# Performance work log

Hardware: AMD Instinct MI355X
Metric: run time of the kernel (lower is better)

Reference implementation:

```python
import jax, jax.numpy as jnp
import numpy as np

NUM_BINS = 64
MAX_DIST = 25.0
HIDDEN = 256
B = 64        # number of graphs
S = 1024      # points per graph (setup builds equal-size contiguous segments)
EPS = 1e-8


def setup_inputs() -> dict:
    key = jax.random.key(0)
    k1, k2, k3, k4, k5 = jax.random.split(key, 5)
    N = B * S
    # scale positions so pairwise distances spread across [0, 25] bins
    pos = jax.random.normal(k1, (N, 3), dtype=jnp.float32) * 5.0
    batch = jnp.repeat(jnp.arange(B, dtype=jnp.int32), S)  # sorted graph ids
    # nn.Linear params, torch convention W:[out,in]
    W1 = jax.random.normal(k2, (HIDDEN, NUM_BINS), dtype=jnp.float32) / np.sqrt(NUM_BINS)
    b1 = jax.random.normal(k3, (HIDDEN,), dtype=jnp.float32) * 0.01
    W2 = jax.random.normal(k4, (HIDDEN, HIDDEN), dtype=jnp.float32) / np.sqrt(HIDDEN)
    b2 = jax.random.normal(k5, (HIDDEN,), dtype=jnp.float32) * 0.01
    return {"pos": pos, "W1": W1, "b1": b1, "W2": W2, "b2": b2, "batch": batch}


def _histograms(pos, batch):
    # batch ids are contiguous equal-size segments -> reshape into [B,S,3]
    p = pos.reshape(B, S, 3)
    # pairwise distances per graph via gram trick (matches torch.cdist)
    sq = jnp.sum(p * p, axis=-1)                                  # [B,S]
    d2 = sq[:, :, None] + sq[:, None, :] - 2.0 * jnp.einsum("bsd,btd->bst", p, p)
    dist = jnp.sqrt(jnp.maximum(d2, 0.0))                         # [B,S,S]
    triu = jnp.triu(jnp.ones((S, S), dtype=bool), k=1)            # i<j pairs
    # histc semantics: values in [0, MAX_DIST] counted, value==MAX_DIST -> last bin
    valid = triu[None] & (dist <= MAX_DIST)
    bins = jnp.clip(jnp.floor(dist * (NUM_BINS / MAX_DIST)).astype(jnp.int32), 0, NUM_BINS - 1)
    ids = (jnp.arange(B, dtype=jnp.int32)[:, None, None] * NUM_BINS + bins).reshape(-1)
    hist = jax.ops.segment_sum(valid.astype(jnp.float32).reshape(-1), ids,
                               num_segments=B * NUM_BINS).reshape(B, NUM_BINS)
    return hist / (jnp.sum(hist, axis=-1, keepdims=True) + EPS)


def reference(pos, W1, b1, W2, b2, batch):
    hist = _histograms(pos, batch)                                # [B, NUM_BINS]
    h = jax.nn.silu(hist @ W1.T + b1)                             # [B, HIDDEN]
    return h @ W2.T + b2                                          # [B, HIDDEN]
```

## Files before the change

### kernel.cpp

```cpp
#include <hip/hip_runtime.h>

#define NBINS 64
#define NGRAPH 64
#define HID 256
#define TILE 128
#define NPAIR 36
#define BPG NPAIR
#define WSUB 16
#define NSUB 64
#define HSTR 65

__device__ __constant__ unsigned char ti_tab[NPAIR] = {
  0,0,0,0,0,0,0,0, 1,1,1,1,1,1,1, 2,2,2,2,2,2, 3,3,3,3,3, 4,4,4,4, 5,5,5, 6,6, 7};
__device__ __constant__ unsigned char tj_tab[NPAIR] = {
  0,1,2,3,4,5,6,7, 1,2,3,4,5,6,7, 2,3,4,5,6,7, 3,4,5,6,7, 4,5,6,7, 5,6,7, 6,7, 7};

template <bool OFFDIAG>
__device__ __forceinline__ void pair_loop(const float4* __restrict__ plj,
                                          unsigned int* __restrict__ hw,
                                          float4 pa, float4 pb, int il0, int il1,
                                          int jbase) {
  #pragma unroll 8
  for (int jj = 0; jj < 32; ++jj) {
    int jl = jbase + jj;
    float4 pj = plj[jl];
    float dxa = pa.x - pj.x, dya = pa.y - pj.y, dza = pa.z - pj.z;
    float d2a = dxa * dxa + dya * dya + dza * dza;
    float dxb = pb.x - pj.x, dyb = pb.y - pj.y, dzb = pb.z - pj.z;
    float d2b = dxb * dxb + dyb * dyb + dzb * dzb;
    unsigned int ia = (unsigned int)(int)__builtin_amdgcn_sqrtf(d2a);
    unsigned int ib = (unsigned int)(int)__builtin_amdgcn_sqrtf(d2b);
    ia = ia > 64u ? 64u : ia;
    ib = ib > 64u ? 64u : ib;
    if (!OFFDIAG) {
      ia = (il0 < jl) ? ia : 64u;
      ib = (il1 < jl) ? ib : 64u;
    }
    atomicAdd(&hw[ia], 1u);
    atomicAdd(&hw[ib], 1u);
  }
}

__global__ __launch_bounds__(256) void hist_kernel(const float* __restrict__ pos,
                                                   unsigned int* __restrict__ partial) {
  int bid = blockIdx.x;
  int g   = bid / NPAIR;
  int p   = bid - g * NPAIR;
  int ti  = ti_tab[p];
  int tj  = tj_tab[p];
  int t   = threadIdx.x;
  const float S = 2.56f;

  __shared__ float4 plj[TILE];
  __shared__ unsigned int h[NSUB * HSTR];

  #pragma unroll
  for (int k = t; k < NSUB * HSTR; k += 256) h[k] = 0u;
  if (t < TILE) {
    const float* gp = pos + (size_t)((g << 10) + (tj << 7) + t) * 3;
    plj[t] = make_float4(gp[0] * S, gp[1] * S, gp[2] * S, 0.0f);
  }

  int il0 = (t & 63) * 2;
  int il1 = il0 + 1;
  const float* ip = pos + (size_t)((g << 10) + (ti << 7) + il0) * 3;
  float4 pa = make_float4(ip[0] * S, ip[1] * S, ip[2] * S, 0.0f);
  float4 pb = make_float4(ip[3] * S, ip[4] * S, ip[5] * S, 0.0f);
  int jbase = (t >> 6) * 32;
  unsigned int* hw = h + ((t >> 6) * WSUB + (t & (WSUB - 1))) * HSTR;
  __syncthreads();

  if (ti != tj) pair_loop<true >(plj, hw, pa, pb, il0, il1, jbase);
  else          pair_loop<false>(plj, hw, pa, pb, il0, il1, jbase);
  __syncthreads();

  if (t < NBINS) {
    unsigned int s = 0u;
    #pragma unroll
    for (int k = 0; k < NSUB; ++k) s += h[k * HSTR + t];
    partial[(size_t)bid * NBINS + t] = s;
  }
}

__global__ __launch_bounds__(256) void mlp_kernel(const unsigned int* __restrict__ partial,
                                                  const float* __restrict__ W1,
                                                  const float* __restrict__ b1,
                                                  const float* __restrict__ W2,
                                                  const float* __restrict__ b2,
                                                  float* __restrict__ out) {
  int g = blockIdx.x >> 2;
  int q = blockIdx.x & 3;
  int t = threadIdx.x;
  __shared__ float hn[NBINS];
  __shared__ float h1[HID];
  __shared__ float p2[4][NBINS];

  if (t < NBINS) {
    unsigned int s = 0u;
    const unsigned int* pp = partial + (size_t)g * BPG * NBINS + t;
    #pragma unroll
    for (int p = 0; p < BPG; ++p) s += pp[p * NBINS];
    float hv = (float)s;
    float tot = hv;
    #pragma unroll
    for (int m = 1; m < 64; m <<= 1) tot += __shfl_xor(tot, m, 64);
    hn[t] = hv / (tot + 1e-8f);
  }
  __syncthreads();

  {
    float acc = b1[t];
    const float4* w = (const float4*)(W1 + (size_t)t * NBINS);
    #pragma unroll
    for (int k = 0; k < NBINS / 4; ++k) {
      float4 wv = w[k];
      acc += hn[4 * k] * wv.x + hn[4 * k + 1] * wv.y +
             hn[4 * k + 2] * wv.z + hn[4 * k + 3] * wv.w;
    }
    float sig = 1.0f / (1.0f + expf(-acc));
    h1[t] = acc * sig;
  }
  __syncthreads();

  {
    int o  = (q << 6) + (t & 63);
    int ks = (t >> 6) << 6;
    float acc = 0.0f;
    const float4* w = (const float4*)(W2 + (size_t)o * HID + ks);
    #pragma unroll
    for (int k = 0; k < 16; ++k) {
      float4 wv = w[k];
      acc += h1[ks + 4 * k] * wv.x + h1[ks + 4 * k + 1] * wv.y +
             h1[ks + 4 * k + 2] * wv.z + h1[ks + 4 * k + 3] * wv.w;
    }
    p2[t >> 6][t & 63] = acc;
  }
  __syncthreads();

  if (t < 64) {
    int o = (q << 6) + t;
    out[(size_t)g * HID + o] = b2[o] + p2[0][t] + p2[1][t] + p2[2][t] + p2[3][t];
  }
}

extern "C" void kernel_launch(void* const* d_in, const int* in_sizes, int n_in,
                              void* d_out, int out_size, void* d_ws, size_t ws_size,
                              hipStream_t stream) {
  const float* pos = (const float*)d_in[0];
  const float* W1  = (const float*)d_in[1];
  const float* b1  = (const float*)d_in[2];
  const float* W2  = (const float*)d_in[3];
  const float* b2  = (const float*)d_in[4];

  unsigned int* partial = (unsigned int*)d_ws;

  hipLaunchKernelGGL(hist_kernel, dim3(NGRAPH * BPG), dim3(256), 0, stream, pos, partial);
  hipLaunchKernelGGL(mlp_kernel, dim3(NGRAPH * 4), dim3(256), 0, stream,
                     partial, W1, b1, W2, b2, (float*)d_out);
}
```

Baseline: 86.32 us.

## Use 256x128 rectangular pair tiles with 4 i-points per thread

The histogram kernel switches from 36 square 128x128 upper-triangle tiles per graph to 20 rectangular tiles of 256 i-points by 128 j-points. Each thread now handles four i-points against each shared j-point, so every LDS load of a j-point is reused more. The i-point loads become three float4 vector loads. The per-block sub-histogram count is halved (32 copies instead of 64), which cuts init and reduction work but may raise atomic contention. The MLP kernel spreads the partial-histogram reduction across all four waves instead of one.

```diff
diff --git a/kernel.cpp b/kernel.cpp
--- a/kernel.cpp
+++ b/kernel.cpp
@@ -3,75 +3,75 @@
 #define NBINS 64
 #define NGRAPH 64
 #define HID 256
-#define TILE 128
-#define NPAIR 36
-#define BPG NPAIR
-#define WSUB 16
-#define NSUB 64
+#define TJ 128
+#define NBLK 20
+#define BPG NBLK
+#define PPW 5
+#define NSUB 32
 #define HSTR 65
 
-__device__ __constant__ unsigned char ti_tab[NPAIR] = {
-  0,0,0,0,0,0,0,0, 1,1,1,1,1,1,1, 2,2,2,2,2,2, 3,3,3,3,3, 4,4,4,4, 5,5,5, 6,6, 7};
-__device__ __constant__ unsigned char tj_tab[NPAIR] = {
-  0,1,2,3,4,5,6,7, 1,2,3,4,5,6,7, 2,3,4,5,6,7, 3,4,5,6,7, 4,5,6,7, 5,6,7, 6,7, 7};
+__device__ __constant__ unsigned char itab[NBLK] = {
+  0,0,0,0,0,0,0,0, 1,1,1,1,1,1, 2,2,2,2, 3,3};
+__device__ __constant__ unsigned char jtab[NBLK] = {
+  0,1,2,3,4,5,6,7, 2,3,4,5,6,7, 4,5,6,7, 6,7};
 
-template <bool OFFDIAG>
+template <bool FULL>
 __device__ __forceinline__ void pair_loop(const float4* __restrict__ plj,
                                           unsigned int* __restrict__ hw,
-                                          float4 pa, float4 pb, int il0, int il1,
-                                          int jbase) {
-  #pragma unroll 8
+                                          const float4* p, int irel, int jbase) {
+  #pragma unroll 4
   for (int jj = 0; jj < 32; ++jj) {
     int jl = jbase + jj;
     float4 pj = plj[jl];
-    float dxa = pa.x - pj.x, dya = pa.y - pj.y, dza = pa.z - pj.z;
-    float d2a = dxa * dxa + dya * dya + dza * dza;
-    float dxb = pb.x - pj.x, dyb = pb.y - pj.y, dzb = pb.z - pj.z;
-    float d2b = dxb * dxb + dyb * dyb + dzb * dzb;
-    unsigned int ia = (unsigned int)(int)__builtin_amdgcn_sqrtf(d2a);
-    unsigned int ib = (unsigned int)(int)__builtin_amdgcn_sqrtf(d2b);
-    ia = ia > 64u ? 64u : ia;
-    ib = ib > 64u ? 64u : ib;
-    if (!OFFDIAG) {
-      ia = (il0 < jl) ? ia : 64u;
-      ib = (il1 < jl) ? ib : 64u;
+    #pragma unroll
+    for (int m = 0; m < 4; ++m) {
+      float dx = p[m].x - pj.x, dy = p[m].y - pj.y, dz = p[m].z - pj.z;
+      float d2 = dx * dx + dy * dy + dz * dz;
+      unsigned int b = (unsigned int)(int)__builtin_amdgcn_sqrtf(d2);
+      b = b > 64u ? 64u : b;
+      if (!FULL) b = (irel + m < jl) ? b : 64u;
+      atomicAdd(&hw[b], 1u);
     }
-    atomicAdd(&hw[ia], 1u);
-    atomicAdd(&hw[ib], 1u);
   }
 }
 
 __global__ __launch_bounds__(256) void hist_kernel(const float* __restrict__ pos,
                                                    unsigned int* __restrict__ partial) {
   int bid = blockIdx.x;
-  int g   = bid / NPAIR;
-  int p   = bid - g * NPAIR;
-  int ti  = ti_tab[p];
-  int tj  = tj_tab[p];
+  int g   = bid / NBLK;
+  int p   = bid - g * NBLK;
+  int ti  = itab[p];
+  int tj  = jtab[p];
+  bool full = (tj >= 2 * ti + 2);
   int t   = threadIdx.x;
   const float S = 2.56f;
 
-  __shared__ float4 plj[TILE];
+  __shared__ float4 plj[TJ];
   __shared__ unsigned int h[NSUB * HSTR];
 
-  #pragma unroll
   for (int k = t; k < NSUB * HSTR; k += 256) h[k] = 0u;
-  if (t < TILE) {
+  if (t < TJ) {
     const float* gp = pos + (size_t)((g << 10) + (tj << 7) + t) * 3;
     plj[t] = make_float4(gp[0] * S, gp[1] * S, gp[2] * S, 0.0f);
   }
 
-  int il0 = (t & 63) * 2;
-  int il1 = il0 + 1;
-  const float* ip = pos + (size_t)((g << 10) + (ti << 7) + il0) * 3;
-  float4 pa = make_float4(ip[0] * S, ip[1] * S, ip[2] * S, 0.0f);
-  float4 pb = make_float4(ip[3] * S, ip[4] * S, ip[5] * S, 0.0f);
+  int il = (t & 63) << 2;
+  const float* ip = pos + (size_t)((g << 10) + (ti << 8) + il) * 3;
+  float4 A = *(const float4*)(ip);
+  float4 Bv = *(const float4*)(ip + 4);
+  float4 C = *(const float4*)(ip + 8);
+  float4 pp[4];
+  pp[0] = make_float4(A.x * S, A.y * S, A.z * S, 0.f);
+  pp[1] = make_float4(A.w * S, Bv.x * S, Bv.y * S, 0.f);
+  pp[2] = make_float4(Bv.z * S, Bv.w * S, C.x * S, 0.f);
+  pp[3] = make_float4(C.y * S, C.z * S, C.w * S, 0.f);
+  int irel  = (ti << 8) + il - (tj << 7);
   int jbase = (t >> 6) * 32;
-  unsigned int* hw = h + ((t >> 6) * WSUB + (t & (WSUB - 1))) * HSTR;
+  unsigned int* hw = h + ((t >> 6) * 8 + (t & 7)) * HSTR;
   __syncthreads();
 
-  if (ti != tj) pair_loop<true >(plj, hw, pa, pb, il0, il1, jbase);
-  else          pair_loop<false>(plj, hw, pa, pb, il0, il1, jbase);
+  if (full) pair_loop<true >(plj, hw, pp, irel, jbase);
+  else      pair_loop<false>(plj, hw, pp, irel, jbase);
   __syncthreads();
 
   if (t < NBINS) {
@@ -91,16 +91,22 @@
   int g = blockIdx.x >> 2;
   int q = blockIdx.x & 3;
   int t = threadIdx.x;
+  int w = t >> 6, l = t & 63;
+  __shared__ float psum[4][NBINS];
   __shared__ float hn[NBINS];
   __shared__ float h1[HID];
   __shared__ float p2[4][NBINS];
 
+  {
+    unsigned int s = 0u;
+    const unsigned int* pp = partial + (size_t)g * BPG * NBINS + l;
+    #pragma unroll
+    for (int k = 0; k < PPW; ++k) s += pp[(w * PPW + k) * NBINS];
+    psum[w][l] = (float)s;
+  }
+  __syncthreads();
   if (t < NBINS) {
-    unsigned int s = 0u;
-    const unsigned int* pp = partial + (size_t)g * BPG * NBINS + t;
-    #pragma unroll
-    for (int p = 0; p < BPG; ++p) s += pp[p * NBINS];
-    float hv = (float)s;
+    float hv = psum[0][t] + psum[1][t] + psum[2][t] + psum[3][t];
     float tot = hv;
     #pragma unroll
     for (int m = 1; m < 64; m <<= 1) tot += __shfl_xor(tot, m, 64);
@@ -110,10 +116,10 @@
 
   {
     float acc = b1[t];
-    const float4* w = (const float4*)(W1 + (size_t)t * NBINS);
+    const float4* wv4 = (const float4*)(W1 + (size_t)t * NBINS);
     #pragma unroll
     for (int k = 0; k < NBINS / 4; ++k) {
-      float4 wv = w[k];
+      float4 wv = wv4[k];
       acc += hn[4 * k] * wv.x + hn[4 * k + 1] * wv.y +
              hn[4 * k + 2] * wv.z + hn[4 * k + 3] * wv.w;
     }
@@ -123,17 +129,17 @@
   __syncthreads();
 
   {
-    int o  = (q << 6) + (t & 63);
-    int ks = (t >> 6) << 6;
+    int o  = (q << 6) + l;
+    int ks = w << 6;
     float acc = 0.0f;
-    const float4* w = (const float4*)(W2 + (size_t)o * HID + ks);
+    const float4* wv4 = (const float4*)(W2 + (size_t)o * HID + ks);
     #pragma unroll
     for (int k = 0; k < 16; ++k) {
-      float4 wv = w[k];
+      float4 wv = wv4[k];
       acc += h1[ks + 4 * k] * wv.x + h1[ks + 4 * k + 1] * wv.y +
              h1[ks + 4 * k + 2] * wv.z + h1[ks + 4 * k + 3] * wv.w;
     }
-    p2[t >> 6][t & 63] = acc;
+    p2[w][l] = acc;
   }
   __syncthreads();
 
@@ -154,7 +160,7 @@
 
   unsigned int* partial = (unsigned int*)d_ws;
 
-  hipLaunchKernelGGL(hist_kernel, dim3(NGRAPH * BPG), dim3(256), 0, stream, pos, partial);
+  hipLaunchKernelGGL(hist_kernel, dim3(NGRAPH * NBLK), dim3(256), 0, stream, pos, partial);
   hipLaunchKernelGGL(mlp_kernel, dim3(NGRAPH * 4), dim3(256), 0, stream,
                      partial, W1, b1, W2, b2, (float*)d_out);
 }
```

After: 86.82 us. No clear change (+0.6%).
